# Kernel tuning notes

Measured on AMD Instinct MI355X. Metric: run time of the kernel, lower is better.

## Reference

```python
import jax, jax.numpy as jnp
import numpy as np

B, C_IN, HW_IN = 32, 3, 262
NUM_CLASSES = 10
GW = 64              # grid side after two conv+pool blocks: 262->260->130->128->64
N_PER = GW * GW      # 4096 nodes per image
N_NODES = B * N_PER  # 131072
E_EDGES = B * 3 * N_PER  # 393216
EPS = 1e-6
BN_EPS = 1e-5


def _build_edges():
    # Faithful replication of CGAT.build_graph edge construction (incl. its odd i*(w-1)+j indexing)
    w = h = GW
    e = []
    for i in range(w):
        for j in range(h):
            a = i * (w - 1) + j
            e.append((a, a))
            e.append((a, a + 1))
            e.append((a, i * w + j))
    e = np.asarray(e, dtype=np.int32)  # [3*n, 2]
    e = e[None, :, :] + (np.arange(B, dtype=np.int32) * N_PER)[:, None, None]
    e = e.reshape(-1, 2)
    return jnp.asarray(e[:, 0]), jnp.asarray(e[:, 1])


def _xavier(key, shape):
    fan_out, fan_in = shape[-2], shape[-1]
    lim = float(np.sqrt(6.0 / (fan_in + fan_out)))
    return jax.random.uniform(key, shape, jnp.float32, -lim, lim)


def setup_inputs() -> dict:
    key = jax.random.key(0)
    ks = iter(jax.random.split(key, 40))
    inp = {}
    inp['x'] = jax.random.normal(next(ks), (B, C_IN, HW_IN, HW_IN), jnp.float32)
    # conv block 1: Conv2d(3,32,3) + BN(32)
    inp['W1'] = jax.random.normal(next(ks), (32, C_IN, 3, 3), jnp.float32) * 0.1
    inp['b1'] = jnp.zeros((32,), jnp.float32)
    inp['g1'] = jnp.ones((32,), jnp.float32)
    inp['be1'] = jnp.zeros((32,), jnp.float32)
    # conv block 2: Conv2d(32,32,3) + BN(32)
    inp['W2'] = jax.random.normal(next(ks), (32, 32, 3, 3), jnp.float32) * 0.05
    inp['b2'] = jnp.zeros((32,), jnp.float32)
    inp['g2'] = jnp.ones((32,), jnp.float32)
    inp['be2'] = jnp.zeros((32,), jnp.float32)
    # GAT layers: sizes [32,32,64,64], heads [1,2,2,2]; head params stacked on leading axis
    # L1: d_in_eff=32 -> d_out=32, 2 heads
    inp['fW1'] = _xavier(next(ks), (2, 32, 64)); inp['fb1'] = jnp.zeros((2, 32), jnp.float32)
    inp['wW1'] = _xavier(next(ks), (2, 1, 64)); inp['wb1'] = jnp.zeros((2, 1), jnp.float32)
    # L2: d_in_eff=64 -> d_out=64, 2 heads
    inp['fW2'] = _xavier(next(ks), (2, 64, 128)); inp['fb2'] = jnp.zeros((2, 64), jnp.float32)
    inp['wW2'] = _xavier(next(ks), (2, 1, 128)); inp['wb2'] = jnp.zeros((2, 1), jnp.float32)
    # L3: d_in_eff=128 -> d_out=64, 2 heads
    inp['fW3'] = _xavier(next(ks), (2, 64, 256)); inp['fb3'] = jnp.zeros((2, 64), jnp.float32)
    inp['wW3'] = _xavier(next(ks), (2, 1, 256)); inp['wb3'] = jnp.zeros((2, 1), jnp.float32)
    # MLP head: [128, 32, num_classes]
    inp['m1W'] = _xavier(next(ks), (32, 128)); inp['m1b'] = jnp.zeros((32,), jnp.float32)
    inp['m2W'] = _xavier(next(ks), (NUM_CLASSES, 32)); inp['m2b'] = jnp.zeros((NUM_CLASSES,), jnp.float32)
    src, tgt = _build_edges()
    inp['src'] = src
    inp['tgt'] = tgt
    inp['graph_id'] = jnp.repeat(jnp.arange(B, dtype=jnp.int32), N_PER)
    return inp


def _conv_block(x, W, b, g, be):
    x = jax.lax.conv_general_dilated(x, W, (1, 1), 'VALID',
                                     dimension_numbers=('NCHW', 'OIHW', 'NCHW'))
    x = x + b[None, :, None, None]
    mu = jnp.mean(x, axis=(0, 2, 3), keepdims=True)       # BatchNorm in training mode
    var = jnp.var(x, axis=(0, 2, 3), keepdims=True)
    x = (x - mu) * jax.lax.rsqrt(var + BN_EPS) * g[None, :, None, None] + be[None, :, None, None]
    x = jax.nn.relu(x)
    return jax.lax.reduce_window(x, -jnp.inf, jax.lax.max, (1, 1, 2, 2), (1, 1, 2, 2), 'VALID')


def _gat_layer(x, src, tgt, fW, fb, wW, wb):
    # x: [N, d_in_eff]; fW: [H, f, 2d]; wW: [H, 1, 2d]
    n = x.shape[0]
    h = jnp.concatenate([x[src], x[tgt]], axis=1)                    # [E, 2d] gather
    y = jax.nn.relu(jnp.einsum('ed,hfd->ehf', h, fW) + fb[None])     # [E, H, f]
    a = jnp.einsum('ed,hod->eho', h, wW) + wb[None]                  # [E, H, 1]
    a_exp = jnp.exp(a - jnp.max(a, axis=0, keepdims=True))           # global max, per head (as torch)
    # Mtgt @ v  ==  segment_sum(v, tgt)  (edge-softmax denominator/numerator)
    a_sum = jax.ops.segment_sum(a_exp, tgt, num_segments=n) + EPS    # [N, H, 1]
    o = jax.ops.segment_sum(y * a_exp, tgt, num_segments=n) / a_sum  # [N, H, f]
    return o.reshape(n, -1)                                          # concat heads


def _forward(x, W1, b1, g1, be1, W2, b2, g2, be2,
             fW1, fb1, wW1, wb1, fW2, fb2, wW2, wb2, fW3, fb3, wW3, wb3,
             m1W, m1b, m2W, m2b, src, tgt, graph_id):
    x = _conv_block(x, W1, b1, g1, be1)
    x = _conv_block(x, W2, b2, g2, be2)   # [B, 32, 64, 64]
    b, c = x.shape[0], x.shape[1]
    x = x.reshape(b, c, -1).transpose(0, 2, 1).reshape(-1, c)  # [N, 32]
    x = _gat_layer(x, src, tgt, fW1, fb1, wW1, wb1)  # [N, 64]
    x = _gat_layer(x, src, tgt, fW2, fb2, wW2, wb2)  # [N, 128]
    x = _gat_layer(x, src, tgt, fW3, fb3, wW3, wb3)  # [N, 128]
    x = jax.ops.segment_sum(x, graph_id, num_segments=B)  # Mgraph^T @ x -> [B, 128]
    x = jax.nn.relu(x @ m1W.T + m1b)
    return x @ m2W.T + m2b


def reference(x, W1, b1, g1, be1, W2, b2, g2, be2,
              fW1, fb1, wW1, wb1, fW2, fb2, wW2, wb2, fW3, fb3, wW3, wb3,
              m1W, m1b, m2W, m2b, src, tgt, graph_id):
    return _forward(x, W1, b1, g1, be1, W2, b2, g2, be2,
                    fW1, fb1, wW1, wb1, fW2, fb2, wW2, wb2, fW3, fb3, wW3, wb3,
                    m1W, m1b, m2W, m2b, src, tgt, graph_id)
```

## Files before the change

### kernel.cpp

```cpp
#include <hip/hip_runtime.h>
#include <math.h>

#define NNODES  131072
#define NEDGES  393216

static const size_t OFF_X     = 0;
static const size_t OFF_U     = 16777216;
static const size_t OFF_PA    = OFF_U + 16777216;
static const size_t OFF_GPOOL = OFF_PA;
static const size_t OFF_V     = OFF_U + 17305600;
static const size_t OFF_AEXP  = OFF_V + 16777216;
static const size_t OFF_CUR   = OFF_AEXP + 786432;
static const size_t OFF_CSRE  = OFF_CUR + 131072;
static const size_t OFF_WUV   = OFF_CSRE + 393216;
static const size_t OFF_UB    = OFF_WUV + 32768;
static const size_t OFF_STATS = OFF_UB + 128;
static const size_t OFF_SS    = OFF_STATS + 128;
static const size_t OFF_AMAX  = OFF_SS + 64;

__device__ inline unsigned enc_f(float f) {
  int b = __float_as_int(f);
  unsigned u = (unsigned)b;
  return (b >= 0) ? (u | 0x80000000u) : ~u;
}
__device__ inline float dec_f(unsigned e) {
  unsigned b = (e & 0x80000000u) ? (e & 0x7FFFFFFFu) : ~e;
  return __int_as_float((int)b);
}

__global__ void repackW1_k(const float* __restrict__ W1, float* __restrict__ W1T) {
  int i = blockIdx.x * 256 + threadIdx.x;
  if (i >= 864) return;
  int j = i >> 5, c = i & 31;
  W1T[i] = W1[c * 27 + j];
}

__global__ void repackW2_k(const float* __restrict__ W2, float* __restrict__ W2T) {
  int i = blockIdx.x * 256 + threadIdx.x;
  if (i >= 9216) return;
  int j = i >> 5, c = i & 31;
  W2T[i] = W2[c * 288 + j];
}

__global__ __launch_bounds__(256) void conv1_tiled_k(const float* __restrict__ x,
    const float* __restrict__ W1T, const float* __restrict__ b1,
    float* __restrict__ PR1, float* __restrict__ part) {
  __shared__ float in_t[972];
  __shared__ float rs1[256], rs2[256];
  int tx = blockIdx.x, ty = blockIdx.y, b = blockIdx.z;
  int tid = threadIdx.x;
  int r0 = 16 * ty, c0 = 16 * tx;
  for (int idx = tid; idx < 972; idx += 256) {
    int ci = idx / 324, rc = idx - ci * 324;
    int row = rc / 18, col = rc - row * 18;
    int gr = r0 + row, gc = c0 + col;
    float v = 0.f;
    if (gr < 262 && gc < 262) v = x[(size_t)(b * 3 + ci) * 68644 + gr * 262 + gc];
    in_t[idx] = v;
  }
  __syncthreads();
  int c = tid & 31, pg = tid >> 5;
  float w[27];
#pragma unroll
  for (int j = 0; j < 27; ++j) w[j] = W1T[j * 32 + c];
  float bias = b1[c];
  int px = tx * 8 + pg;
  float s1 = 0.f, s2 = 0.f;
#pragma unroll
  for (int r = 0; r < 8; ++r) {
    int py = ty * 8 + r;
    if (py < 130 && px < 130) {
      float a00 = bias, a01 = bias, a10 = bias, a11 = bias;
#pragma unroll
      for (int ci = 0; ci < 3; ++ci) {
        const float* ip = &in_t[ci * 324 + (2 * r) * 18 + 2 * pg];
#pragma unroll
        for (int dy = 0; dy < 3; ++dy) {
#pragma unroll
          for (int dx = 0; dx < 3; ++dx) {
            float wv = w[ci * 9 + dy * 3 + dx];
            a00 += ip[dy * 18 + dx]           * wv;
            a01 += ip[dy * 18 + dx + 1]       * wv;
            a10 += ip[(dy + 1) * 18 + dx]     * wv;
            a11 += ip[(dy + 1) * 18 + dx + 1] * wv;
          }
        }
      }
      s1 += a00 + a01 + a10 + a11;
      s2 += a00 * a00 + a01 * a01 + a10 * a10 + a11 * a11;
      float m = fmaxf(fmaxf(a00, a01), fmaxf(a10, a11));
      PR1[((size_t)b * 16900 + py * 130 + px) * 32 + c] = m;
    }
  }
  rs1[tid] = s1; rs2[tid] = s2;
  __syncthreads();
  if (tid < 32) {
    float a = 0.f, q = 0.f;
    for (int g = 0; g < 8; ++g) { a += rs1[g * 32 + tid]; q += rs2[g * 32 + tid]; }
    int bid = (b * 17 + ty) * 17 + tx;
    part[(size_t)bid * 64 + tid * 2 + 0] = a;
    part[(size_t)bid * 64 + tid * 2 + 1] = q;
  }
}

__global__ void stats_reduce_k(const float* __restrict__ part, double* __restrict__ stats, int nb) {
  __shared__ double sd[256];
  int cnt = blockIdx.x;
  double s = 0.0;
  for (int b = threadIdx.x; b < nb; b += 256) s += (double)part[(size_t)b * 64 + cnt];
  sd[threadIdx.x] = s;
  __syncthreads();
  for (int o = 128; o > 0; o >>= 1) { if (threadIdx.x < o) sd[threadIdx.x] += sd[threadIdx.x + o]; __syncthreads(); }
  if (threadIdx.x == 0) stats[cnt] = sd[0];
}

__global__ void bn_finalize_k(const double* __restrict__ stats, const float* __restrict__ g,
                              const float* __restrict__ be, float* __restrict__ ss, double inv_cnt) {
  int c = threadIdx.x;
  if (c < 32) {
    double mu  = stats[c * 2 + 0] * inv_cnt;
    double var = stats[c * 2 + 1] * inv_cnt - mu * mu;
    double scale = (double)g[c] / sqrt(var + 1e-5);
    ss[c]      = (float)scale;
    ss[32 + c] = (float)((double)be[c] - mu * scale);
  }
}

__global__ void bn_relu1_k(float* __restrict__ PR1, const float* __restrict__ ss) {
  int i = blockIdx.x * 256 + threadIdx.x;
  int c = i & 31;
  PR1[i] = fmaxf(PR1[i] * ss[c] + ss[32 + c], 0.f);
}

__global__ __launch_bounds__(256) void conv2_tiled_k(const float* __restrict__ pool1,
    const float* __restrict__ W2T, const float* __restrict__ b2,
    float* __restrict__ PR2, float* __restrict__ part) {
  __shared__ float in_t[10368];
  __shared__ float rs1[256], rs2[256];
  int tx = blockIdx.x, ty = blockIdx.y, b = blockIdx.z;
  int tid = threadIdx.x;
  int r0 = 16 * ty, c0 = 16 * tx;
  const float* pb = pool1 + ((size_t)b * 16900 + r0 * 130 + c0) * 32;
  for (int idx = tid; idx < 10368; idx += 256) {
    int rc = idx >> 5, ci = idx & 31;
    int row = rc / 18, col = rc - row * 18;
    in_t[idx] = pb[(size_t)(row * 130 + col) * 32 + ci];
  }
  __syncthreads();
  int c = tid & 31, pg = tid >> 5;
  float bias = b2[c];
  float acc[8][4];
#pragma unroll
  for (int r = 0; r < 8; ++r) { acc[r][0] = bias; acc[r][1] = bias; acc[r][2] = bias; acc[r][3] = bias; }
  int cb = 2 * pg;
  float w[9], wn[9];
#pragma unroll
  for (int k = 0; k < 9; ++k) w[k] = W2T[k * 32 + c];
#pragma unroll 1
  for (int ci = 0; ci < 32; ++ci) {
    if (ci < 31) {
#pragma unroll
      for (int k = 0; k < 9; ++k) wn[k] = W2T[((ci + 1) * 9 + k) * 32 + c];
    }
    float r0v[4], r1v[4], r2v[4], r3v[4];
#pragma unroll
    for (int q = 0; q < 4; ++q) {
      r0v[q] = in_t[(0 * 18 + cb + q) * 32 + ci];
      r1v[q] = in_t[(1 * 18 + cb + q) * 32 + ci];
    }
#pragma unroll
    for (int r = 0; r < 8; ++r) {
#pragma unroll
      for (int q = 0; q < 4; ++q) {
        r2v[q] = in_t[((2 * r + 2) * 18 + cb + q) * 32 + ci];
        r3v[q] = in_t[((2 * r + 3) * 18 + cb + q) * 32 + ci];
      }
#pragma unroll
      for (int dx = 0; dx < 3; ++dx) {
        float w0 = w[dx], w1 = w[3 + dx], w2 = w[6 + dx];
        acc[r][0] += r0v[dx]     * w0 + r1v[dx]     * w1 + r2v[dx]     * w2;
        acc[r][1] += r0v[dx + 1] * w0 + r1v[dx + 1] * w1 + r2v[dx + 1] * w2;
        acc[r][2] += r1v[dx]     * w0 + r2v[dx]     * w1 + r3v[dx]     * w2;
        acc[r][3] += r1v[dx + 1] * w0 + r2v[dx + 1] * w1 + r3v[dx + 1] * w2;
      }
#pragma unroll
      for (int q = 0; q < 4; ++q) { r0v[q] = r2v[q]; r1v[q] = r3v[q]; }
    }
#pragma unroll
    for (int k = 0; k < 9; ++k) w[k] = wn[k];
  }
  float s1 = 0.f, s2 = 0.f;
  int px = tx * 8 + pg;
#pragma unroll
  for (int r = 0; r < 8; ++r) {
    s1 += acc[r][0] + acc[r][1] + acc[r][2] + acc[r][3];
    s2 += acc[r][0] * acc[r][0] + acc[r][1] * acc[r][1] + acc[r][2] * acc[r][2] + acc[r][3] * acc[r][3];
    int py = ty * 8 + r;
    float m = fmaxf(fmaxf(acc[r][0], acc[r][1]), fmaxf(acc[r][2], acc[r][3]));
    PR2[((size_t)b * 4096 + py * 64 + px) * 32 + c] = m;
  }
  rs1[tid] = s1; rs2[tid] = s2;
  __syncthreads();
  if (tid < 32) {
    float a = 0.f, q = 0.f;
    for (int g = 0; g < 8; ++g) { a += rs1[g * 32 + tid]; q += rs2[g * 32 + tid]; }
    int bid = (b * 8 + ty) * 8 + tx;
    part[(size_t)bid * 64 + tid * 2 + 0] = a;
    part[(size_t)bid * 64 + tid * 2 + 1] = q;
  }
}

__global__ void bn_relu2_k(const float* __restrict__ PR2, const float* __restrict__ ss,
                           float* __restrict__ X) {
  int i = blockIdx.x * 256 + threadIdx.x;
  int c = i & 31;
  X[i] = fmaxf(PR2[i] * ss[c] + ss[32 + c], 0.f);
}

__global__ void deg_k(const int* __restrict__ tgt, int* __restrict__ cur) {
  int e = blockIdx.x * 256 + threadIdx.x;
  atomicAdd(&cur[tgt[e]], 1);
}

__global__ void scan_k(int* __restrict__ cur) {
  __shared__ int ls[1024];
  int tid = threadIdx.x;
  int base = tid * 128;
  int sum = 0;
  for (int i = 0; i < 128; ++i) sum += cur[base + i];
  ls[tid] = sum;
  __syncthreads();
  for (int off = 1; off < 1024; off <<= 1) {
    int v = (tid >= off) ? ls[tid - off] : 0;
    __syncthreads();
    ls[tid] += v;
    __syncthreads();
  }
  int excl = ls[tid] - sum;
  for (int i = 0; i < 128; ++i) { int d = cur[base + i]; cur[base + i] = excl; excl += d; }
}

__global__ void scatter_k(const int* __restrict__ tgt, int* __restrict__ cur,
                          int* __restrict__ csre) {
  int e = blockIdx.x * 256 + threadIdx.x;
  int t = tgt[e];
  int pos = atomicAdd(&cur[t], 1);
  csre[pos] = e;
}

__global__ void repack2_k(const float* __restrict__ fW, const float* __restrict__ fb,
                          float* __restrict__ WUV, float* __restrict__ UB,
                          unsigned* __restrict__ amax, int D, int HF) {
  int NN = 2 * HF, D2 = 2 * D;
  int i = blockIdx.x * 256 + threadIdx.x;
  if (i < 2) amax[i] = 0x007FFFFFu;
  if (i < HF) UB[i] = fb[i];
  if (i >= D * NN) return;
  int k = i / NN, j = i - k * NN;
  int half = (j >= HF) ? 1 : 0;
  int cc = j - half * HF;
  WUV[i] = fW[(size_t)cc * D2 + half * D + k];
}

__global__ __launch_bounds__(256) void gemm_uv_k(const float* __restrict__ X,
    const float* __restrict__ WUV, const float* __restrict__ UB,
    float* __restrict__ U, float* __restrict__ V, int D, int HF) {
  const int NN = 2 * HF;
  __shared__ float As[16][68];
  __shared__ float Bs[16][68];
  int tid = threadIdx.x;
  int tx = tid & 15, ty = tid >> 4;
  int rm = blockIdx.y * 64;
  int cn = blockIdx.x * 64;
  float acc[4][4] = {};
  int ar = tid >> 2;
  int ak = (tid & 3) * 4;
  int bk = tid >> 4;
  int bj = (tid & 15) * 4;
  for (int kb = 0; kb < D; kb += 16) {
    float4 av = *(const float4*)&X[(size_t)(rm + ar) * D + kb + ak];
    float4 bv = *(const float4*)&WUV[(size_t)(kb + bk) * NN + cn + bj];
    __syncthreads();
    As[ak + 0][ar] = av.x; As[ak + 1][ar] = av.y; As[ak + 2][ar] = av.z; As[ak + 3][ar] = av.w;
    *(float4*)&Bs[bk][bj] = bv;
    __syncthreads();
#pragma unroll
    for (int k = 0; k < 16; ++k) {
      float4 a = *(float4*)&As[k][ty * 4];
      float4 b = *(float4*)&Bs[k][tx * 4];
      acc[0][0] += a.x * b.x; acc[0][1] += a.x * b.y; acc[0][2] += a.x * b.z; acc[0][3] += a.x * b.w;
      acc[1][0] += a.y * b.x; acc[1][1] += a.y * b.y; acc[1][2] += a.y * b.z; acc[1][3] += a.y * b.w;
      acc[2][0] += a.z * b.x; acc[2][1] += a.z * b.y; acc[2][2] += a.z * b.z; acc[2][3] += a.z * b.w;
      acc[3][0] += a.w * b.x; acc[3][1] += a.w * b.y; acc[3][2] += a.w * b.z; acc[3][3] += a.w * b.w;
    }
  }
  bool isU = (cn < HF);
  float4 ub = make_float4(0.f, 0.f, 0.f, 0.f);
  if (isU) ub = *(const float4*)&UB[cn + tx * 4];
  float* dstBase = isU ? (U + cn) : (V + (cn - HF));
#pragma unroll
  for (int i = 0; i < 4; ++i) {
    int row = rm + ty * 4 + i;
    float4 o = make_float4(acc[i][0] + ub.x, acc[i][1] + ub.y, acc[i][2] + ub.z, acc[i][3] + ub.w);
    *(float4*)&dstBase[(size_t)row * HF + tx * 4] = o;
  }
}

__global__ void pvec_k(const float* __restrict__ X, const float* __restrict__ wW,
                       const float* __restrict__ wb, float* __restrict__ PA, int D) {
  __shared__ float PWs[4 * 132];
  int tid = threadIdx.x;
  int D2 = 2 * D;
  for (int i = tid; i < 4 * D; i += 64) {
    int v = i / D, k = i - v * D;
    PWs[v * 132 + k] = (v < 2) ? wW[v * D2 + k] : wW[(v - 2) * D2 + D + k];
  }
  __syncthreads();
  int v = tid & 3;
  int n = blockIdx.x * 16 + (tid >> 2);
  const float* xr = X + (size_t)n * D;
  float acc = 0.f;
  for (int k = 0; k < D; k += 4) {
    float4 xv = *(const float4*)&xr[k];
    acc += xv.x * PWs[v * 132 + k] + xv.y * PWs[v * 132 + k + 1]
         + xv.z * PWs[v * 132 + k + 2] + xv.w * PWs[v * 132 + k + 3];
  }
  if (v < 2) acc += wb[v];
  PA[(size_t)n * 4 + v] = acc;
}

__global__ void edge_logit_k(const int* __restrict__ src, const int* __restrict__ tgt,
                             const float* __restrict__ PA, float* __restrict__ aexp,
                             unsigned* __restrict__ amax) {
  int e = blockIdx.x * 256 + threadIdx.x;
  int s = src[e], t = tgt[e];
  float4 ps = *(const float4*)&PA[(size_t)s * 4];
  float4 pt = *(const float4*)&PA[(size_t)t * 4];
  float a0 = ps.x + pt.z;
  float a1 = ps.y + pt.w;
  aexp[e * 2 + 0] = a0;
  aexp[e * 2 + 1] = a1;
#pragma unroll
  for (int o = 32; o > 0; o >>= 1) {
    a0 = fmaxf(a0, __shfl_down(a0, o));
    a1 = fmaxf(a1, __shfl_down(a1, o));
  }
  if ((threadIdx.x & 63) == 0) {
    atomicMax(&amax[0], enc_f(a0));
    atomicMax(&amax[1], enc_f(a1));
  }
}

__global__ void edge_exp_k(float* __restrict__ aexp, const unsigned* __restrict__ amax) {
  int e = blockIdx.x * 256 + threadIdx.x;
  float m0 = dec_f(amax[0]), m1 = dec_f(amax[1]);
  float2 lg = *(float2*)&aexp[e * 2];
  lg.x = __expf(lg.x - m0);
  lg.y = __expf(lg.y - m1);
  *(float2*)&aexp[e * 2] = lg;
}

__global__ void gather_k(const int* __restrict__ cur, const int* __restrict__ csre,
                         const int* __restrict__ src, const float* __restrict__ aexp,
                         const float* __restrict__ U, const float* __restrict__ V,
                         float* __restrict__ X, int HF, int F, int lq) {
  int tid = blockIdx.x * 256 + threadIdx.x;
  int r4 = tid & ((HF >> 2) - 1);
  int t = tid >> lq;
  int r0 = r4 << 2;
  int h = (r0 >= F) ? 1 : 0;
  int start = (t == 0) ? 0 : cur[t - 1];
  int end = cur[t];
  float4 v4 = *(const float4*)&V[(size_t)t * HF + r0];
  float ax = 0.f, ay = 0.f, az = 0.f, aw = 0.f, den = 0.f;
  for (int e = start; e < end; ++e) {
    int eo = csre[e];
    int s = src[eo];
    float ae = aexp[(size_t)eo * 2 + h];
    den += ae;
    const float4 u4 = *(const float4*)&U[(size_t)s * HF + r0];
    ax += ae * fmaxf(u4.x + v4.x, 0.f);
    ay += ae * fmaxf(u4.y + v4.y, 0.f);
    az += ae * fmaxf(u4.z + v4.z, 0.f);
    aw += ae * fmaxf(u4.w + v4.w, 0.f);
  }
  float inv = 1.f / (den + 1e-6f);
  float4 o = make_float4(ax * inv, ay * inv, az * inv, aw * inv);
  *(float4*)&X[(size_t)t * HF + r0] = o;
}

__global__ void graph_pool_k(const float* __restrict__ X, float* __restrict__ gp) {
  int g = blockIdx.y, chunk = blockIdx.x, j = threadIdx.x;
  int base = g * 4096 + chunk * 128;
  float acc = 0.f;
  for (int i = 0; i < 128; ++i) acc += X[(size_t)(base + i) * 128 + j];
  atomicAdd(&gp[g * 128 + j], acc);
}

__global__ void mlp_k(const float* __restrict__ gp, const float* __restrict__ m1W,
                      const float* __restrict__ m1b, const float* __restrict__ m2W,
                      const float* __restrict__ m2b, float* __restrict__ out) {
  __shared__ float hid[1024];
  int tid = threadIdx.x;
  int g = tid >> 5, j = tid & 31;
  float acc = m1b[j];
  for (int k = 0; k < 128; ++k) acc += gp[g * 128 + k] * m1W[j * 128 + k];
  hid[g * 32 + j] = fmaxf(acc, 0.f);
  __syncthreads();
  if (tid < 320) {
    int gg = tid / 10, c2 = tid - gg * 10;
    float o = m2b[c2];
    for (int k = 0; k < 32; ++k) o += hid[gg * 32 + k] * m2W[c2 * 32 + k];
    out[gg * 10 + c2] = o;
  }
}

extern "C" void kernel_launch(void* const* d_in, const int* in_sizes, int n_in,
                              void* d_out, int out_size, void* d_ws, size_t ws_size,
                              hipStream_t stream) {
  (void)in_sizes; (void)n_in; (void)out_size; (void)ws_size;
  const float* x   = (const float*)d_in[0];
  const float* W1  = (const float*)d_in[1];
  const float* b1  = (const float*)d_in[2];
  const float* g1  = (const float*)d_in[3];
  const float* be1 = (const float*)d_in[4];
  const float* W2  = (const float*)d_in[5];
  const float* b2  = (const float*)d_in[6];
  const float* g2  = (const float*)d_in[7];
  const float* be2 = (const float*)d_in[8];
  const int* src = (const int*)d_in[25];
  const int* tgt = (const int*)d_in[26];

  float* ws = (float*)d_ws;
  float* X     = ws + OFF_X;
  float* PR1   = ws + OFF_U;
  float* U     = ws + OFF_U;
  float* V     = ws + OFF_V;
  float* AEXP  = ws + OFF_AEXP;
  float* PA    = ws + OFF_PA;
  int*   CUR   = (int*)(ws + OFF_CUR);
  int*   CSRE  = (int*)(ws + OFF_CSRE);
  float* WUV   = ws + OFF_WUV;
  float* UB    = ws + OFF_UB;
  double* STATS= (double*)(ws + OFF_STATS);
  float* SS    = ws + OFF_SS;
  float* GPOOL = ws + OFF_GPOOL;
  unsigned* AMAX = (unsigned*)(ws + OFF_AMAX);
  float* PART  = X;
  float* W1T   = X + 1000000;
  float* W2T   = X + 1001000;

  repackW1_k<<<4, 256, 0, stream>>>(W1, W1T);
  repackW2_k<<<36, 256, 0, stream>>>(W2, W2T);

  conv1_tiled_k<<<dim3(17, 17, 32), 256, 0, stream>>>(x, W1T, b1, PR1, PART);
  stats_reduce_k<<<64, 256, 0, stream>>>(PART, STATS, 9248);
  bn_finalize_k<<<1, 64, 0, stream>>>(STATS, g1, be1, SS, 1.0 / 2163200.0);
  bn_relu1_k<<<67600, 256, 0, stream>>>(PR1, SS);

  conv2_tiled_k<<<dim3(8, 8, 32), 256, 0, stream>>>(PR1, W2T, b2, V, PART);
  stats_reduce_k<<<64, 256, 0, stream>>>(PART, STATS, 2048);
  bn_finalize_k<<<1, 64, 0, stream>>>(STATS, g2, be2, SS, 1.0 / 524288.0);
  bn_relu2_k<<<16384, 256, 0, stream>>>(V, SS, X);

  hipMemsetAsync(CUR, 0, NNODES * sizeof(int), stream);
  deg_k<<<NEDGES / 256, 256, 0, stream>>>(tgt, CUR);
  scan_k<<<1, 1024, 0, stream>>>(CUR);
  scatter_k<<<NEDGES / 256, 256, 0, stream>>>(tgt, CUR, CSRE);

  for (int l = 0; l < 3; ++l) {
    int D  = (l == 0) ? 32 : (l == 1) ? 64 : 128;
    int F  = (l == 0) ? 32 : 64;
    int HF = 2 * F, NN = 2 * HF;
    int lq = (l == 0) ? 4 : 5;
    const float* fW = (const float*)d_in[9  + l * 4];
    const float* fb = (const float*)d_in[10 + l * 4];
    const float* wW = (const float*)d_in[11 + l * 4];
    const float* wb = (const float*)d_in[12 + l * 4];

    repack2_k<<<(D * NN + 255) / 256, 256, 0, stream>>>(fW, fb, WUV, UB, AMAX, D, HF);
    gemm_uv_k<<<dim3(NN / 64, NNODES / 64), 256, 0, stream>>>(X, WUV, UB, U, V, D, HF);
    pvec_k<<<NNODES / 16, 64, 0, stream>>>(X, wW, wb, PA, D);
    edge_logit_k<<<NEDGES / 256, 256, 0, stream>>>(src, tgt, PA, AEXP, AMAX);
    edge_exp_k<<<NEDGES / 256, 256, 0, stream>>>(AEXP, AMAX);
    gather_k<<<(NNODES * (HF / 4)) / 256, 256, 0, stream>>>(CUR, CSRE, src, AEXP, U, V, X, HF, F, lq);
  }

  hipMemsetAsync(GPOOL, 0, 4096 * sizeof(float), stream);
  graph_pool_k<<<dim3(32, 32), 128, 0, stream>>>(X, GPOOL);
  mlp_k<<<1, 1024, 0, stream>>>(GPOOL, (const float*)d_in[21], (const float*)d_in[22],
                                (const float*)d_in[23], (const float*)d_in[24], (float*)d_out);
}
```

Before: 1.346 ms.

## Fuse BN1+ReLU into conv2 tile load and enlarge GEMM row tile

The separate bn_relu1 pass over the pooled conv1 output is removed, and the scale/shift plus ReLU is applied while conv2 loads its input tile into shared memory. This saves a full read and write of a roughly 69 MB buffer and one launch. Separately, the UV GEMM now computes 128 rows per block (8x4 outputs per thread) instead of 64, which improves reuse of the B tile and halves the block count at the cost of more registers per thread. Halo elements are normalized several times across neighbouring tiles, which is cheap.

```diff
diff --git a/kernel.cpp b/kernel.cpp
--- a/kernel.cpp
+++ b/kernel.cpp
@@ -126,25 +126,23 @@
   }
 }
 
-__global__ void bn_relu1_k(float* __restrict__ PR1, const float* __restrict__ ss) {
-  int i = blockIdx.x * 256 + threadIdx.x;
-  int c = i & 31;
-  PR1[i] = fmaxf(PR1[i] * ss[c] + ss[32 + c], 0.f);
-}
-
 __global__ __launch_bounds__(256) void conv2_tiled_k(const float* __restrict__ pool1,
-    const float* __restrict__ W2T, const float* __restrict__ b2,
+    const float* __restrict__ ss, const float* __restrict__ W2T, const float* __restrict__ b2,
     float* __restrict__ PR2, float* __restrict__ part) {
   __shared__ float in_t[10368];
   __shared__ float rs1[256], rs2[256];
+  __shared__ float ssl[64];
   int tx = blockIdx.x, ty = blockIdx.y, b = blockIdx.z;
   int tid = threadIdx.x;
+  if (tid < 64) ssl[tid] = ss[tid];
+  __syncthreads();
   int r0 = 16 * ty, c0 = 16 * tx;
   const float* pb = pool1 + ((size_t)b * 16900 + r0 * 130 + c0) * 32;
   for (int idx = tid; idx < 10368; idx += 256) {
     int rc = idx >> 5, ci = idx & 31;
     int row = rc / 18, col = rc - row * 18;
-    in_t[idx] = pb[(size_t)(row * 130 + col) * 32 + ci];
+    float v = pb[(size_t)(row * 130 + col) * 32 + ci];
+    in_t[idx] = fmaxf(v * ssl[ci] + ssl[32 + ci], 0.f);
   }
   __syncthreads();
   int c = tid & 31, pg = tid >> 5;
@@ -266,32 +264,40 @@
     const float* __restrict__ WUV, const float* __restrict__ UB,
     float* __restrict__ U, float* __restrict__ V, int D, int HF) {
   const int NN = 2 * HF;
-  __shared__ float As[16][68];
+  __shared__ float As[16][132];
   __shared__ float Bs[16][68];
   int tid = threadIdx.x;
   int tx = tid & 15, ty = tid >> 4;
-  int rm = blockIdx.y * 64;
+  int rm = blockIdx.y * 128;
   int cn = blockIdx.x * 64;
-  float acc[4][4] = {};
-  int ar = tid >> 2;
-  int ak = (tid & 3) * 4;
+  float acc[8][4] = {};
+  int ar = tid >> 1;
+  int ak = (tid & 1) * 8;
   int bk = tid >> 4;
   int bj = (tid & 15) * 4;
   for (int kb = 0; kb < D; kb += 16) {
-    float4 av = *(const float4*)&X[(size_t)(rm + ar) * D + kb + ak];
+    const float* xr = &X[(size_t)(rm + ar) * D + kb + ak];
+    float4 a0 = *(const float4*)&xr[0];
+    float4 a1 = *(const float4*)&xr[4];
     float4 bv = *(const float4*)&WUV[(size_t)(kb + bk) * NN + cn + bj];
     __syncthreads();
-    As[ak + 0][ar] = av.x; As[ak + 1][ar] = av.y; As[ak + 2][ar] = av.z; As[ak + 3][ar] = av.w;
+    As[ak + 0][ar] = a0.x; As[ak + 1][ar] = a0.y; As[ak + 2][ar] = a0.z; As[ak + 3][ar] = a0.w;
+    As[ak + 4][ar] = a1.x; As[ak + 5][ar] = a1.y; As[ak + 6][ar] = a1.z; As[ak + 7][ar] = a1.w;
     *(float4*)&Bs[bk][bj] = bv;
     __syncthreads();
 #pragma unroll
     for (int k = 0; k < 16; ++k) {
-      float4 a = *(float4*)&As[k][ty * 4];
+      float4 am0 = *(float4*)&As[k][ty * 8];
+      float4 am1 = *(float4*)&As[k][ty * 8 + 4];
       float4 b = *(float4*)&Bs[k][tx * 4];
-      acc[0][0] += a.x * b.x; acc[0][1] += a.x * b.y; acc[0][2] += a.x * b.z; acc[0][3] += a.x * b.w;
-      acc[1][0] += a.y * b.x; acc[1][1] += a.y * b.y; acc[1][2] += a.y * b.z; acc[1][3] += a.y * b.w;
-      acc[2][0] += a.z * b.x; acc[2][1] += a.z * b.y; acc[2][2] += a.z * b.z; acc[2][3] += a.z * b.w;
-      acc[3][0] += a.w * b.x; acc[3][1] += a.w * b.y; acc[3][2] += a.w * b.z; acc[3][3] += a.w * b.w;
+      acc[0][0] += am0.x * b.x; acc[0][1] += am0.x * b.y; acc[0][2] += am0.x * b.z; acc[0][3] += am0.x * b.w;
+      acc[1][0] += am0.y * b.x; acc[1][1] += am0.y * b.y; acc[1][2] += am0.y * b.z; acc[1][3] += am0.y * b.w;
+      acc[2][0] += am0.z * b.x; acc[2][1] += am0.z * b.y; acc[2][2] += am0.z * b.z; acc[2][3] += am0.z * b.w;
+      acc[3][0] += am0.w * b.x; acc[3][1] += am0.w * b.y; acc[3][2] += am0.w * b.z; acc[3][3] += am0.w * b.w;
+      acc[4][0] += am1.x * b.x; acc[4][1] += am1.x * b.y; acc[4][2] += am1.x * b.z; acc[4][3] += am1.x * b.w;
+      acc[5][0] += am1.y * b.x; acc[5][1] += am1.y * b.y; acc[5][2] += am1.y * b.z; acc[5][3] += am1.y * b.w;
+      acc[6][0] += am1.z * b.x; acc[6][1] += am1.z * b.y; acc[6][2] += am1.z * b.z; acc[6][3] += am1.z * b.w;
+      acc[7][0] += am1.w * b.x; acc[7][1] += am1.w * b.y; acc[7][2] += am1.w * b.z; acc[7][3] += am1.w * b.w;
     }
   }
   bool isU = (cn < HF);
@@ -299,8 +305,8 @@
   if (isU) ub = *(const float4*)&UB[cn + tx * 4];
   float* dstBase = isU ? (U + cn) : (V + (cn - HF));
 #pragma unroll
-  for (int i = 0; i < 4; ++i) {
-    int row = rm + ty * 4 + i;
+  for (int i = 0; i < 8; ++i) {
+    int row = rm + ty * 8 + i;
     float4 o = make_float4(acc[i][0] + ub.x, acc[i][1] + ub.y, acc[i][2] + ub.z, acc[i][3] + ub.w);
     *(float4*)&dstBase[(size_t)row * HF + tx * 4] = o;
   }
@@ -456,9 +462,8 @@
   conv1_tiled_k<<<dim3(17, 17, 32), 256, 0, stream>>>(x, W1T, b1, PR1, PART);
   stats_reduce_k<<<64, 256, 0, stream>>>(PART, STATS, 9248);
   bn_finalize_k<<<1, 64, 0, stream>>>(STATS, g1, be1, SS, 1.0 / 2163200.0);
-  bn_relu1_k<<<67600, 256, 0, stream>>>(PR1, SS);
-
-  conv2_tiled_k<<<dim3(8, 8, 32), 256, 0, stream>>>(PR1, W2T, b2, V, PART);
+
+  conv2_tiled_k<<<dim3(8, 8, 32), 256, 0, stream>>>(PR1, SS, W2T, b2, V, PART);
   stats_reduce_k<<<64, 256, 0, stream>>>(PART, STATS, 2048);
   bn_finalize_k<<<1, 64, 0, stream>>>(STATS, g2, be2, SS, 1.0 / 524288.0);
   bn_relu2_k<<<16384, 256, 0, stream>>>(V, SS, X);
@@ -479,7 +484,7 @@
     const float* wb = (const float*)d_in[12 + l * 4];
 
     repack2_k<<<(D * NN + 255) / 256, 256, 0, stream>>>(fW, fb, WUV, UB, AMAX, D, HF);
-    gemm_uv_k<<<dim3(NN / 64, NNODES / 64), 256, 0, stream>>>(X, WUV, UB, U, V, D, HF);
+    gemm_uv_k<<<dim3(NN / 64, NNODES / 128), 256, 0, stream>>>(X, WUV, UB, U, V, D, HF);
     pvec_k<<<NNODES / 16, 64, 0, stream>>>(X, wW, wb, PA, D);
     edge_logit_k<<<NEDGES / 256, 256, 0, stream>>>(src, tgt, PA, AEXP, AMAX);
     edge_exp_k<<<NEDGES / 256, 256, 0, stream>>>(AEXP, AMAX);
```

Measured after the change: 1.309 ms. 2.8% less time.
